# Kernel optimization log

Hardware: AMD Instinct MI355X
Metric: run time of the kernel (lower is better)

Reference implementation:

```python
import jax, jax.numpy as jnp
import numpy as np

EPS = 1e-5
KH = KW = 3
PAD = 1

def conv3x3(x, w, b=None):
    out = jax.lax.conv_general_dilated(
        x, w, window_strides=(1, 1), padding=((PAD, PAD), (PAD, PAD)),
        dimension_numbers=("NCHW", "OIHW", "NCHW"))
    if b is not None:
        out = out + b[None, :, None, None]
    return out

def batchnorm(x, gamma, beta):
    # training-mode BatchNorm2d: batch statistics over (N, H, W)
    mean = x.mean(axis=(0, 2, 3), keepdims=True)
    var = x.var(axis=(0, 2, 3), keepdims=True)
    return gamma[None, :, None, None] * (x - mean) / jnp.sqrt(var + EPS) + beta[None, :, None, None]

def bilinear_gather(x, y_pos, x_pos):
    # x: [B,C,H,W]; y_pos/x_pos: [B,P,H,W] (P = KH*KW sampling taps)
    # zero padding outside image (mmcv modulated deform conv semantics)
    B, C, H, W = x.shape
    P = y_pos.shape[1]
    x_flat = x.reshape(B, C, H * W)
    y0 = jnp.floor(y_pos)
    x0 = jnp.floor(x_pos)
    ly = y_pos - y0
    lx = x_pos - x0
    out = jnp.zeros((B, C, P, H, W), dtype=x.dtype)
    for dy, dx, wgt in ((0, 0, (1 - ly) * (1 - lx)), (0, 1, (1 - ly) * lx),
                        (1, 0, ly * (1 - lx)), (1, 1, ly * lx)):
        yi = y0 + dy
        xi = x0 + dx
        valid = ((yi >= 0) & (yi <= H - 1) & (xi >= 0) & (xi <= W - 1)).astype(x.dtype)
        yc = jnp.clip(yi, 0, H - 1).astype(jnp.int32)
        xc = jnp.clip(xi, 0, W - 1).astype(jnp.int32)
        idx = (yc * W + xc).reshape(B, 1, P * H * W)
        vals = jnp.take_along_axis(x_flat, jnp.broadcast_to(idx, (B, C, P * H * W)), axis=2)
        vals = vals.reshape(B, C, P, H, W)
        out = out + vals * (wgt * valid)[:, None]
    return out  # [B,C,P,H,W]

def modulated_deform_conv(x, w_off, b_off, w_dcn):
    B, C, H, W = x.shape
    P = KH * KW
    off = conv3x3(x, w_off, b_off)  # [B, 3*P, H, W]
    o1, o2, m = jnp.split(off, 3, axis=1)
    offset = jnp.concatenate([o1, o2], axis=1)            # [B, 2P, H, W]
    offset = offset.reshape(B, P, 2, H, W)                # channel 2p -> dy, 2p+1 -> dx
    mask = jax.nn.sigmoid(m)                              # [B, P, H, W]
    hh = jnp.arange(H, dtype=x.dtype)
    ww = jnp.arange(W, dtype=x.dtype)
    ky = jnp.arange(KH, dtype=x.dtype)
    kx = jnp.arange(KW, dtype=x.dtype)
    # base sampling grid per tap p = ky*KW + kx: (h - PAD + ky, w - PAD + kx)
    base_y = (hh[None, :] - PAD + ky[:, None])            # [KH, H]
    base_x = (ww[None, :] - PAD + kx[:, None])            # [KW, W]
    base_y = jnp.broadcast_to(base_y[:, None, :, None], (KH, KW, H, W)).reshape(P, H, W)
    base_x = jnp.broadcast_to(base_x[None, :, None, :], (KH, KW, H, W)).reshape(P, H, W)
    y_pos = base_y[None] + offset[:, :, 0]                # [B,P,H,W]
    x_pos = base_x[None] + offset[:, :, 1]
    sampled = bilinear_gather(x, y_pos, x_pos)            # [B,C,P,H,W]
    sampled = sampled * mask[:, None]
    w = w_dcn.reshape(w_dcn.shape[0], C, P)               # [O, C, P]
    return jnp.einsum("bcphw,ocp->bohw", sampled, w)

def setup_inputs() -> dict:
    key = jax.random.key(0)
    ks = jax.random.split(key, 10)
    B, Ch, H, W = 4, 256, 64, 64
    Cin, Cout = 2 * Ch, 256
    P = KH * KW
    inp = {
        "input_v": jax.random.normal(ks[0], (B, Ch, H, W), jnp.float32),
        "input_i": jax.random.normal(ks[1], (B, Ch, H, W), jnp.float32),
        "w_off": jax.random.normal(ks[2], (3 * P, Cin, KH, KW), jnp.float32) * 0.01,
        "b_off": jnp.zeros((3 * P,), jnp.float32),
        "w_dcn": jax.random.normal(ks[3], (Cout, Cin, KH, KW), jnp.float32) * (1.0 / np.sqrt(Cin * P)),
        "gamma1": jnp.ones((Cout,), jnp.float32),
        "beta1": jnp.zeros((Cout,), jnp.float32),
        "w2": jax.random.normal(ks[4], (Cout, Cout, KH, KW), jnp.float32) * (1.0 / np.sqrt(Cout * P)),
        "gamma2": jnp.ones((Cout,), jnp.float32),
        "beta2": jnp.zeros((Cout,), jnp.float32),
    }
    return inp

def reference(input_v, input_i, w_off, b_off, w_dcn, gamma1, beta1, w2, gamma2, beta2):
    x = jnp.concatenate([input_v, input_i], axis=1)
    out = modulated_deform_conv(x, w_off, b_off, w_dcn)
    out = jax.nn.relu(batchnorm(out, gamma1, beta1))
    out = jax.nn.relu(batchnorm(conv3x3(out, w2), gamma2, beta2))
    return out
```

## Files before the change

kernel.cpp:

```cpp
#include <hip/hip_runtime.h>
#include <cstdint>
#include <cstddef>

typedef unsigned short u16;
typedef __attribute__((ext_vector_type(8))) short s16x8;
typedef __attribute__((ext_vector_type(4))) float f32x4;

#define DEV __device__ __forceinline__

DEV float bf2f(short u){
  union { unsigned int i; float f; } v;
  v.i = ((unsigned int)(u16)u) << 16;
  return v.f;
}
DEV short f2bf(float f){
  union { float f; unsigned int i; } v; v.f = f;
  unsigned int u = v.i;
  u += 0x7fffu + ((u >> 16) & 1u);
  return (short)(u >> 16);
}
DEV f32x4 f32x4_zero(){
  f32x4 z;
#pragma unroll
  for(int j=0;j<4;j++) z[j]=0.f;
  return z;
}
DEV f32x4 mfma16(s16x8 a, s16x8 b, f32x4 c){
  return __builtin_amdgcn_mfma_f32_16x16x32_bf16(a, b, c, 0, 0, 0);
}
DEV void bar_lds(){
  asm volatile("s_waitcnt lgkmcnt(0)" ::: "memory");
  __builtin_amdgcn_s_barrier();
}
DEV void gload16(const u16* g, u16* l){
  __builtin_amdgcn_global_load_lds(
      (const __attribute__((address_space(1))) unsigned int*)g,
      (__attribute__((address_space(3))) unsigned int*)l, 16, 0, 0);
}

static constexpr size_t STATS_B     = 0;
static constexpr size_t OUT2_ACC_B  = 4096;
static constexpr size_t XN_PAD_B    = 16781312;
static constexpr size_t OUT1N_PAD_B = 34738176;
static constexpr size_t ZERO_BYTES  = 43659264;
static constexpr size_t OUT1_ACC_B  = 43659264;
static constexpr size_t PPIX_B      = 60436480;
static constexpr size_t PWGT_B      = 62795776;
static constexpr size_t Y_B         = 65155072;
static constexpr size_t WALL_B      = 159428608;
static constexpr size_t W2T_B       = 162181120;

__global__ void k_x_to_nhwc(const float* __restrict__ v, const float* __restrict__ vi,
                            u16* __restrict__ xn){
  __shared__ float tile[64][65];
  const int b = blockIdx.z, c0 = blockIdx.y*64, hw0 = blockIdx.x*64;
  const int h = hw0 >> 6;
  const float* src = (c0 < 256) ? (v  + ((size_t)b*256 + c0)      *4096)
                                : (vi + ((size_t)b*256 + (c0-256))*4096);
  const int t = threadIdx.x;
#pragma unroll
  for(int k=0;k<16;k++){
    int idx = t + k*256;
    int cl = idx >> 6, wl = idx & 63;
    tile[cl][wl] = src[(size_t)cl*4096 + hw0 + wl];
  }
  __syncthreads();
#pragma unroll
  for(int k=0;k<16;k++){
    int idx = t + k*256;
    int wl = idx >> 6, cl = idx & 63;
    xn[((size_t)(b*66 + h+1)*66 + wl+1)*512 + c0 + cl] = (u16)f2bf(tile[cl][wl]);
  }
}

__global__ void k_prep_wall(const float* __restrict__ wdcn, const float* __restrict__ woff,
                            u16* __restrict__ wt){
  int idx = blockIdx.x*256 + threadIdx.x;
  if(idx >= 2688*512) return;
  int n = idx >> 9, c = idx & 511;
  float val = 0.f;
  if(n < 2304){
    int p = n >> 8, o = n & 255;
    val = wdcn[(size_t)(o*512 + c)*9 + p];
  } else if(n < 2592){
    int q = n - 2304, p = q >> 5, nn = q & 31;
    if(nn < 27) val = woff[(size_t)(nn*512 + c)*9 + p];
  }
  wt[idx] = (u16)f2bf(val);
}
__global__ void k_prep_w2(const float* __restrict__ w, u16* __restrict__ wt){
  int idx = blockIdx.x*256 + threadIdx.x;
  if(idx >= 256*2304) return;
  int n = idx / 2304, k = idx % 2304;
  int t = k >> 8, c = k & 255;
  wt[idx] = (u16)f2bf(w[(size_t)(n*256 + c)*9 + t]);
}

__global__ __launch_bounds__(256, 2) void k_gemm_big(
    const u16* __restrict__ A, const u16* __restrict__ wt, u16* __restrict__ Y){
  const int bid = blockIdx.x;
  const int xcd = bid & 7;
  const int j   = bid >> 3;
  const int mt  = xcd + 8*(j/7);
  const int ng  = j % 7;
  if(mt >= 137) return;
  __shared__ short A_lds[2][8][128][8];
  __shared__ short B_lds[2][8][128][8];
  const int tid = threadIdx.x;
  const int lane = tid & 63, wid = tid >> 6;
  const int quad = lane >> 4, ln = lane & 15;
  const int wm = wid >> 1, wn = wid & 1;
  const int m0 = mt * 128;
  constexpr int NPH = 24;
  f32x4 acc[4][4];
#pragma unroll
  for(int mf=0;mf<4;mf++)
#pragma unroll
    for(int nf=0;nf<4;nf++) acc[mf][nf] = f32x4_zero();

  auto stage = [&](int p, int bi){
    const int n0 = (ng*3 + (p >> 3)) * 128;
    const int k0 = (p & 7) * 64;
#pragma unroll
    for(int i=0;i<4;i++){
      const int idx = wid*4 + i;
      const int s = idx >> 1, rh = (idx & 1)*64;
      gload16(A  + (size_t)(m0 + rh + lane)*512 + k0 + s*8, (u16*)&A_lds[bi][s][rh][0]);
      gload16(wt + (size_t)(n0 + rh + lane)*512 + k0 + s*8, (u16*)&B_lds[bi][s][rh][0]);
    }
  };
  auto compute = [&](int bi){
#pragma unroll
    for(int kk=0;kk<2;kk++){
      s16x8 af[4], bf[4];
#pragma unroll
      for(int mf=0;mf<4;mf++)
        af[mf] = *(const s16x8*)&A_lds[bi][kk*4+quad][wm*64 + mf*16 + ln][0];
#pragma unroll
      for(int nf=0;nf<4;nf++)
        bf[nf] = *(const s16x8*)&B_lds[bi][kk*4+quad][wn*64 + nf*16 + ln][0];
#pragma unroll
      for(int mf=0;mf<4;mf++)
#pragma unroll
        for(int nf=0;nf<4;nf++)
          acc[mf][nf] = mfma16(af[mf], bf[nf], acc[mf][nf]);
    }
  };
  auto flushY = [&](int pass){
    const int n0 = (ng*3 + pass) * 128;
#pragma unroll
    for(int mf=0;mf<4;mf++)
#pragma unroll
      for(int nf=0;nf<4;nf++){
        const int col = n0 + wn*64 + nf*16 + ln;
#pragma unroll
        for(int i=0;i<4;i++){
          const int row = m0 + wm*64 + mf*16 + quad*4 + i;
          Y[(size_t)row*2688 + col] = (u16)f2bf(acc[mf][nf][i]);
        }
        acc[mf][nf] = f32x4_zero();
      }
  };

  stage(0, 0);
  asm volatile("s_waitcnt vmcnt(0)" ::: "memory");
  __builtin_amdgcn_s_barrier();
  stage(1, 1);
  for(int p = 0; p < NPH; ++p){
    const int bi = p & 1;
    compute(bi);
    bar_lds();
    const bool boundary = (p & 7) == 7;
    if(boundary) flushY(p >> 3);
    if(p + 2 < NPH) stage(p + 2, bi);
    if(boundary || p + 2 >= NPH){
      asm volatile("s_waitcnt vmcnt(0)" ::: "memory");
    } else {
      asm volatile("s_waitcnt vmcnt(8)" ::: "memory");
    }
    __builtin_amdgcn_sched_barrier(0);
    __builtin_amdgcn_s_barrier();
  }
}

__global__ __launch_bounds__(256) void k_off_combine(
    const u16* __restrict__ Y, const float* __restrict__ boff,
    int* __restrict__ ppix, float* __restrict__ pwgt){
  __shared__ float offs[64][32];
  const int t = threadIdx.x;
  const int b = blockIdx.x >> 6, h = blockIdx.x & 63;
  const int w = t >> 2, g = t & 3;
  float acc[8];
#pragma unroll
  for(int j=0;j<8;j++) acc[j] = 0.f;
  for(int p=0;p<9;p++){
    const int pp = (b*66 + h + p/3)*66 + (w + p%3);
    s16x8 v = *(const s16x8*)(Y + (size_t)pp*2688 + 2304 + p*32 + g*8);
#pragma unroll
    for(int j=0;j<8;j++) acc[j] += bf2f(v[j]);
  }
#pragma unroll
  for(int j=0;j<8;j++) offs[w][g*8 + j] = acc[j];
  __syncthreads();
  for(int id = t; id < 576; id += 256){
    const int tp = id / 64, ww = id & 63;
    const int m = (b<<12) + (h<<6) + ww;
    float dy = offs[ww][2*tp]   + boff[2*tp];
    float dx = offs[ww][2*tp+1] + boff[2*tp+1];
    float mz = offs[ww][18+tp]  + boff[18+tp];
    float mk = 1.f / (1.f + expf(-mz));
    float ypos = (float)(h - 1 + tp/3) + dy;
    float xpos = (float)(ww - 1 + tp%3) + dx;
    float y0f = floorf(ypos), x0f = floorf(xpos);
    float ly = ypos - y0f, lx = xpos - x0f;
    int y0 = (int)y0f, x0 = (int)x0f;
    const int id4 = (m*9 + tp)*4;
#pragma unroll
    for(int k=0;k<4;k++){
      int ddy = k >> 1, ddx = k & 1;
      int yi = y0 + ddy, xi = x0 + ddx;
      int yc = yi < -1 ? -1 : (yi > 64 ? 64 : yi);
      int xc = xi < -1 ? -1 : (xi > 64 ? 64 : xi);
      float wk = (ddy ? ly : 1.f-ly) * (ddx ? lx : 1.f-lx) * mk;
      ppix[id4+k] = (b*66 + yc+1)*66 + xc+1;
      pwgt[id4+k] = wk;
    }
  }
}

__global__ __launch_bounds__(512) void k_combine(
    const u16* __restrict__ Y, const int* __restrict__ ppix,
    const float* __restrict__ pwgt, float* __restrict__ out1,
    float* __restrict__ sum1, float* __restrict__ sq1){
  __shared__ int   s_pp[64][9][4];
  __shared__ float s_wg[64][9][4];
  __shared__ float s_red[2][8][256];
  const int t = threadIdx.x;
  const int b = blockIdx.x >> 6, h = blockIdx.x & 63;
  const int m_row = (b<<12) + (h<<6);
  for(int id = t; id < 576; id += 512){
    const int mo = id / 9, tp = id - mo*9;
    const size_t i4 = ((size_t)(m_row + mo)*9 + tp)*4;
    int4   pp4 = *(const int4*)  (ppix + i4);
    float4 wg4 = *(const float4*)(pwgt + i4);
    s_pp[mo][tp][0] = pp4.x; s_pp[mo][tp][1] = pp4.y;
    s_pp[mo][tp][2] = pp4.z; s_pp[mo][tp][3] = pp4.w;
    s_wg[mo][tp][0] = wg4.x; s_wg[mo][tp][1] = wg4.y;
    s_wg[mo][tp][2] = wg4.z; s_wg[mo][tp][3] = wg4.w;
  }
  __syncthreads();
  const int wv = t >> 6, lane = t & 63;
  const int c0 = lane*4;
  const int pw0 = wv*8;
  float acc[8][4];
#pragma unroll
  for(int pw=0;pw<8;pw++)
#pragma unroll
    for(int j=0;j<4;j++) acc[pw][j] = 0.f;

  for(int tp = 0; tp < 9; ++tp){
    const int cb = tp*256 + c0;
#pragma unroll
    for(int pw=0;pw<8;pw++){
      const int px = pw0 + pw;
#pragma unroll
      for(int k=0;k<4;k++){
        const float wk = s_wg[px][tp][k];
        const int   pp = s_pp[px][tp][k];
        ushort4 v = *(const ushort4*)(Y + (size_t)pp*2688 + cb);
        acc[pw][0] = fmaf(wk, bf2f((short)v.x), acc[pw][0]);
        acc[pw][1] = fmaf(wk, bf2f((short)v.y), acc[pw][1]);
        acc[pw][2] = fmaf(wk, bf2f((short)v.z), acc[pw][2]);
        acc[pw][3] = fmaf(wk, bf2f((short)v.w), acc[pw][3]);
      }
    }
  }
  float ls[4] = {0.f,0.f,0.f,0.f}, lq[4] = {0.f,0.f,0.f,0.f};
#pragma unroll
  for(int pw=0;pw<8;pw++){
    float4 o4;
    o4.x = acc[pw][0]; o4.y = acc[pw][1]; o4.z = acc[pw][2]; o4.w = acc[pw][3];
    *(float4*)(out1 + (size_t)(m_row + pw0 + pw)*256 + c0) = o4;
#pragma unroll
    for(int j=0;j<4;j++){
      ls[j] += acc[pw][j];
      lq[j] = fmaf(acc[pw][j], acc[pw][j], lq[j]);
    }
  }
#pragma unroll
  for(int j=0;j<4;j++){
    s_red[0][wv][c0+j] = ls[j];
    s_red[1][wv][c0+j] = lq[j];
  }
  __syncthreads();
  if(t < 256){
    float S = 0.f, Q = 0.f;
#pragma unroll
    for(int w8=0;w8<8;w8++){ S += s_red[0][w8][t]; Q += s_red[1][w8][t]; }
    unsafeAtomicAdd(sum1 + t, S);
    unsafeAtomicAdd(sq1 + t, Q);
  }
}

__global__ __launch_bounds__(256, 2) void k_gemm2(
    const u16* __restrict__ a_pad, const u16* __restrict__ wt, float* __restrict__ outa){
  const int bid = blockIdx.x;
  const int xcd = bid & 7;
  const int j   = bid >> 3;
  const int mt  = xcd + 8*(j >> 2);
  const int rest = j & 3;
  const int nt  = rest & 1;
  const int kz  = rest >> 1;
  __shared__ short A_lds[2][8][128][8];
  __shared__ short B_lds[2][8][128][8];
  const int tid = threadIdx.x;
  const int lane = tid & 63, wid = tid >> 6;
  const int quad = lane >> 4, ln = lane & 15;
  const int wm = wid >> 1, wn = wid & 1;
  const int m0 = mt * 128;
  const int n0 = nt * 128;
  const int kbase = kz * 1152;
  const int b = m0 >> 12;
  const int h0 = (m0 & 4095) >> 6;
  constexpr int NPH = 18;
  f32x4 acc[4][4];
#pragma unroll
  for(int mf=0;mf<4;mf++)
#pragma unroll
    for(int nf=0;nf<4;nf++) acc[mf][nf] = f32x4_zero();

  auto stage = [&](int t, int bi){
    const int k0 = kbase + t*64;
    const int tp = k0 >> 8, cit = k0 & 255;
    const int ty = tp/3, tx = tp - ty*3;
#pragma unroll
    for(int i=0;i<4;i++){
      const int idx = wid*4 + i;
      const int s = idx >> 1, rh = (idx & 1)*64;
      const int hh = h0 + (rh >> 6) + ty;
      gload16(a_pad + ((size_t)(b*66 + hh)*66 + lane + tx)*256 + cit + s*8,
              (u16*)&A_lds[bi][s][rh][0]);
      gload16(wt + (size_t)(n0 + rh + lane)*2304 + k0 + s*8,
              (u16*)&B_lds[bi][s][rh][0]);
    }
  };
  auto compute = [&](int bi){
#pragma unroll
    for(int kk=0;kk<2;kk++){
      s16x8 af[4], bf[4];
#pragma unroll
      for(int mf=0;mf<4;mf++)
        af[mf] = *(const s16x8*)&A_lds[bi][kk*4+quad][wm*64 + mf*16 + ln][0];
#pragma unroll
      for(int nf=0;nf<4;nf++)
        bf[nf] = *(const s16x8*)&B_lds[bi][kk*4+quad][wn*64 + nf*16 + ln][0];
#pragma unroll
      for(int mf=0;mf<4;mf++)
#pragma unroll
        for(int nf=0;nf<4;nf++)
          acc[mf][nf] = mfma16(af[mf], bf[nf], acc[mf][nf]);
    }
  };

  stage(0, 0);
  asm volatile("s_waitcnt vmcnt(0)" ::: "memory");
  __builtin_amdgcn_s_barrier();
  stage(1, 1);
  for(int t = 0; t < NPH; ++t){
    const int bi = t & 1;
    compute(bi);
    bar_lds();
    if(t + 2 < NPH){
      stage(t + 2, bi);
      asm volatile("s_waitcnt vmcnt(8)" ::: "memory");
    } else {
      asm volatile("s_waitcnt vmcnt(0)" ::: "memory");
    }
    __builtin_amdgcn_sched_barrier(0);
    __builtin_amdgcn_s_barrier();
  }

#pragma unroll
  for(int mf=0;mf<4;mf++)
#pragma unroll
    for(int nf=0;nf<4;nf++){
      const int col = n0 + wn*64 + nf*16 + ln;
#pragma unroll
      for(int i=0;i<4;i++){
        const int row = m0 + wm*64 + mf*16 + quad*4 + i;
        unsafeAtomicAdd(outa + (size_t)row*256 + col, acc[mf][nf][i]);
      }
    }
}

__global__ void k_stats(const float* __restrict__ acc, float* __restrict__ sum,
                        float* __restrict__ sq){
  const int m0 = blockIdx.x*64;
  const int c = threadIdx.x;
  float s = 0.f, q = 0.f;
  for(int i=0;i<64;i++){
    float v = acc[(size_t)(m0+i)*256 + c];
    s += v; q += v*v;
  }
  unsafeAtomicAdd(sum + c, s);
  unsafeAtomicAdd(sq + c, q);
}

__global__ void k_bn1(const float* __restrict__ acc, const float* __restrict__ sum,
                      const float* __restrict__ sq, const float* __restrict__ g,
                      const float* __restrict__ bt, u16* __restrict__ o){
  __shared__ float sc[256], sh[256];
  const int t = threadIdx.x;
  {
    float mean = sum[t] * (1.f/16384.f);
    float var  = sq[t] * (1.f/16384.f) - mean*mean;
    float rstd = rsqrtf(var + 1e-5f);
    float s = g[t] * rstd;
    sc[t] = s; sh[t] = bt[t] - mean*s;
  }
  __syncthreads();
  const int c4 = (t & 63) * 4;
  const float s0 = sc[c4], s1 = sc[c4+1], s2 = sc[c4+2], s3 = sc[c4+3];
  const float h0 = sh[c4], h1 = sh[c4+1], h2 = sh[c4+2], h3 = sh[c4+3];
#pragma unroll
  for(int k=0;k<4;k++){
    int m = blockIdx.x*16 + k*4 + (t>>6);
    int b = m >> 12, hh = (m >> 6) & 63, ww = m & 63;
    const float4 v = *(const float4*)(acc + (size_t)m*256 + c4);
    unsigned int lo = (unsigned int)(u16)f2bf(fmaxf(0.f, v.x*s0 + h0))
                    | ((unsigned int)(u16)f2bf(fmaxf(0.f, v.y*s1 + h1)) << 16);
    unsigned int hi = (unsigned int)(u16)f2bf(fmaxf(0.f, v.z*s2 + h2))
                    | ((unsigned int)(u16)f2bf(fmaxf(0.f, v.w*s3 + h3)) << 16);
    uint2 pr; pr.x = lo; pr.y = hi;
    *(uint2*)(o + ((size_t)(b*66 + hh+1)*66 + ww+1)*256 + c4) = pr;
  }
}

__global__ void k_bn2_out(const float* __restrict__ acc, const float* __restrict__ sum,
                          const float* __restrict__ sq, const float* __restrict__ g,
                          const float* __restrict__ bt, float* __restrict__ out){
  __shared__ float tile[64][65];
  __shared__ float sc[64], sh[64];
  const int t = threadIdx.x;
  const int b = blockIdx.z, c0 = blockIdx.y*64, hw0 = blockIdx.x*64;
  if(t < 64){
    int c = c0 + t;
    float mean = sum[c] * (1.f/16384.f);
    float var  = sq[c] * (1.f/16384.f) - mean*mean;
    float rstd = rsqrtf(var + 1e-5f);
    float s = g[c] * rstd;
    sc[t] = s; sh[t] = bt[c] - mean*s;
  }
  __syncthreads();
#pragma unroll
  for(int k=0;k<16;k++){
    int idx = t + k*256;
    int wl = idx >> 6, cl = idx & 63;
    float v = acc[(size_t)((b<<12) + hw0 + wl)*256 + c0 + cl];
    tile[wl][cl] = fmaxf(0.f, v*sc[cl] + sh[cl]);
  }
  __syncthreads();
#pragma unroll
  for(int k=0;k<16;k++){
    int idx = t + k*256;
    int cl = idx >> 6, wl = idx & 63;
    out[(size_t)(b*256 + c0 + cl)*4096 + hw0 + wl] = tile[wl][cl];
  }
}

extern "C" void kernel_launch(void* const* d_in, const int* in_sizes, int n_in,
                              void* d_out, int out_size, void* d_ws, size_t ws_size,
                              hipStream_t stream){
  const float* in_v  = (const float*)d_in[0];
  const float* in_i  = (const float*)d_in[1];
  const float* w_off = (const float*)d_in[2];
  const float* b_off = (const float*)d_in[3];
  const float* w_dcn = (const float*)d_in[4];
  const float* g1    = (const float*)d_in[5];
  const float* bt1   = (const float*)d_in[6];
  const float* w2    = (const float*)d_in[7];
  const float* g2    = (const float*)d_in[8];
  const float* bt2   = (const float*)d_in[9];
  float* out = (float*)d_out;
  char* ws = (char*)d_ws;

  float* stats     = (float*)(ws + STATS_B);
  float* out2_acc  = (float*)(ws + OUT2_ACC_B);
  u16*   xn_pad    = (u16*)  (ws + XN_PAD_B);
  u16*   out1n_pad = (u16*)  (ws + OUT1N_PAD_B);
  float* out1_acc  = (float*)(ws + OUT1_ACC_B);
  int*   ppix      = (int*)  (ws + PPIX_B);
  float* pwgt      = (float*)(ws + PWGT_B);
  u16*   Ymat      = (u16*)  (ws + Y_B);
  u16*   wall      = (u16*)  (ws + WALL_B);
  u16*   w2t       = (u16*)  (ws + W2T_B);
  float* sum1 = stats,       *sq1 = stats + 256;
  float* sum2 = stats + 512, *sq2 = stats + 768;

  hipMemsetAsync(ws, 0, ZERO_BYTES, stream);
  k_x_to_nhwc<<<dim3(64,8,4), 256, 0, stream>>>(in_v, in_i, xn_pad);
  k_prep_wall<<<5376, 256, 0, stream>>>(w_dcn, w_off, wall);
  k_prep_w2<<<2304, 256, 0, stream>>>(w2, w2t);
  k_gemm_big<<<1008, 256, 0, stream>>>(xn_pad, wall, Ymat);
  k_off_combine<<<256, 256, 0, stream>>>(Ymat, b_off, ppix, pwgt);
  k_combine<<<256, 512, 0, stream>>>(Ymat, ppix, pwgt, out1_acc, sum1, sq1);
  k_bn1<<<1024, 256, 0, stream>>>(out1_acc, sum1, sq1, g1, bt1, out1n_pad);
  k_gemm2<<<512, 256, 0, stream>>>(out1n_pad, w2t, out2_acc);
  k_stats<<<256, 256, 0, stream>>>(out2_acc, sum2, sq2);
  k_bn2_out<<<dim3(64,4,4), 256, 0, stream>>>(out2_acc, sum2, sq2, g2, bt2, out);
}
```

Baseline: 351.2 us.

## Drop double-buffered pipelines in GEMMs for smaller LDS and higher occupancy

Both GEMM kernels lose their hand-built double-buffered global-to-LDS pipeline and become a simple single-buffer loop: load a K=32 slice, barrier, run the MFMAs, barrier. LDS per block shrinks so launch bounds can request 4 blocks per CU. The big GEMM also drops its multi-pass N loop per block and gives each block a single 128-wide N tile, tripling the grid. The aim is to hide latency through more resident waves instead of explicit prefetch, at the cost of two barriers per smaller K step and no load/compute overlap within a block.

```diff
diff --git a/kernel.cpp b/kernel.cpp
--- a/kernel.cpp
+++ b/kernel.cpp
@@ -27,10 +27,6 @@
 }
 DEV f32x4 mfma16(s16x8 a, s16x8 b, f32x4 c){
   return __builtin_amdgcn_mfma_f32_16x16x32_bf16(a, b, c, 0, 0, 0);
-}
-DEV void bar_lds(){
-  asm volatile("s_waitcnt lgkmcnt(0)" ::: "memory");
-  __builtin_amdgcn_s_barrier();
 }
 DEV void gload16(const u16* g, u16* l){
   __builtin_amdgcn_global_load_lds(
@@ -96,91 +92,68 @@
   wt[idx] = (u16)f2bf(w[(size_t)(n*256 + c)*9 + t]);
 }
 
-__global__ __launch_bounds__(256, 2) void k_gemm_big(
+__global__ __launch_bounds__(256, 4) void k_gemm_big(
     const u16* __restrict__ A, const u16* __restrict__ wt, u16* __restrict__ Y){
   const int bid = blockIdx.x;
   const int xcd = bid & 7;
   const int j   = bid >> 3;
-  const int mt  = xcd + 8*(j/7);
-  const int ng  = j % 7;
+  const int mt  = xcd + 8*(j/21);
+  const int nt  = j % 21;
   if(mt >= 137) return;
-  __shared__ short A_lds[2][8][128][8];
-  __shared__ short B_lds[2][8][128][8];
+  __shared__ short A_lds[4][128][8];
+  __shared__ short B_lds[4][128][8];
   const int tid = threadIdx.x;
   const int lane = tid & 63, wid = tid >> 6;
   const int quad = lane >> 4, ln = lane & 15;
   const int wm = wid >> 1, wn = wid & 1;
   const int m0 = mt * 128;
-  constexpr int NPH = 24;
+  const int n0 = nt * 128;
   f32x4 acc[4][4];
 #pragma unroll
   for(int mf=0;mf<4;mf++)
 #pragma unroll
     for(int nf=0;nf<4;nf++) acc[mf][nf] = f32x4_zero();
 
-  auto stage = [&](int p, int bi){
-    const int n0 = (ng*3 + (p >> 3)) * 128;
-    const int k0 = (p & 7) * 64;
+  for(int t = 0; t < 16; ++t){
+    const int k0 = t*32;
 #pragma unroll
     for(int i=0;i<4;i++){
-      const int idx = wid*4 + i;
-      const int s = idx >> 1, rh = (idx & 1)*64;
-      gload16(A  + (size_t)(m0 + rh + lane)*512 + k0 + s*8, (u16*)&A_lds[bi][s][rh][0]);
-      gload16(wt + (size_t)(n0 + rh + lane)*512 + k0 + s*8, (u16*)&B_lds[bi][s][rh][0]);
-    }
-  };
-  auto compute = [&](int bi){
-#pragma unroll
-    for(int kk=0;kk<2;kk++){
+      const int piece = wid*4 + i;
+      const int s = (piece >> 1) & 3, rh = (piece & 1)*64;
+      if(piece < 8)
+        gload16(A  + (size_t)(m0 + rh + lane)*512 + k0 + s*8, (u16*)&A_lds[s][rh][0]);
+      else
+        gload16(wt + (size_t)(n0 + rh + lane)*512 + k0 + s*8, (u16*)&B_lds[s][rh][0]);
+    }
+    __syncthreads();
+    {
       s16x8 af[4], bf[4];
 #pragma unroll
       for(int mf=0;mf<4;mf++)
-        af[mf] = *(const s16x8*)&A_lds[bi][kk*4+quad][wm*64 + mf*16 + ln][0];
+        af[mf] = *(const s16x8*)&A_lds[quad][wm*64 + mf*16 + ln][0];
 #pragma unroll
       for(int nf=0;nf<4;nf++)
-        bf[nf] = *(const s16x8*)&B_lds[bi][kk*4+quad][wn*64 + nf*16 + ln][0];
+        bf[nf] = *(const s16x8*)&B_lds[quad][wn*64 + nf*16 + ln][0];
 #pragma unroll
       for(int mf=0;mf<4;mf++)
 #pragma unroll
         for(int nf=0;nf<4;nf++)
           acc[mf][nf] = mfma16(af[mf], bf[nf], acc[mf][nf]);
     }
-  };
-  auto flushY = [&](int pass){
-    const int n0 = (ng*3 + pass) * 128;
-#pragma unroll
-    for(int mf=0;mf<4;mf++)
-#pragma unroll
-      for(int nf=0;nf<4;nf++){
-        const int col = n0 + wn*64 + nf*16 + ln;
-#pragma unroll
-        for(int i=0;i<4;i++){
-          const int row = m0 + wm*64 + mf*16 + quad*4 + i;
-          Y[(size_t)row*2688 + col] = (u16)f2bf(acc[mf][nf][i]);
-        }
-        acc[mf][nf] = f32x4_zero();
+    __syncthreads();
+  }
+
+#pragma unroll
+  for(int mf=0;mf<4;mf++)
+#pragma unroll
+    for(int nf=0;nf<4;nf++){
+      const int col = n0 + wn*64 + nf*16 + ln;
+#pragma unroll
+      for(int i=0;i<4;i++){
+        const int row = m0 + wm*64 + mf*16 + quad*4 + i;
+        Y[(size_t)row*2688 + col] = (u16)f2bf(acc[mf][nf][i]);
       }
-  };
-
-  stage(0, 0);
-  asm volatile("s_waitcnt vmcnt(0)" ::: "memory");
-  __builtin_amdgcn_s_barrier();
-  stage(1, 1);
-  for(int p = 0; p < NPH; ++p){
-    const int bi = p & 1;
-    compute(bi);
-    bar_lds();
-    const bool boundary = (p & 7) == 7;
-    if(boundary) flushY(p >> 3);
-    if(p + 2 < NPH) stage(p + 2, bi);
-    if(boundary || p + 2 >= NPH){
-      asm volatile("s_waitcnt vmcnt(0)" ::: "memory");
-    } else {
-      asm volatile("s_waitcnt vmcnt(8)" ::: "memory");
-    }
-    __builtin_amdgcn_sched_barrier(0);
-    __builtin_amdgcn_s_barrier();
-  }
+    }
 }
 
 __global__ __launch_bounds__(256) void k_off_combine(
@@ -302,7 +275,7 @@
   }
 }
 
-__global__ __launch_bounds__(256, 2) void k_gemm2(
+__global__ __launch_bounds__(256, 4) void k_gemm2(
     const u16* __restrict__ a_pad, const u16* __restrict__ wt, float* __restrict__ outa){
   const int bid = blockIdx.x;
   const int xcd = bid & 7;
@@ -311,8 +284,8 @@
   const int rest = j & 3;
   const int nt  = rest & 1;
   const int kz  = rest >> 1;
-  __shared__ short A_lds[2][8][128][8];
-  __shared__ short B_lds[2][8][128][8];
+  __shared__ short A_lds[4][128][8];
+  __shared__ short B_lds[4][128][8];
   const int tid = threadIdx.x;
   const int lane = tid & 63, wid = tid >> 6;
   const int quad = lane >> 4, ln = lane & 15;
@@ -322,62 +295,45 @@
   const int kbase = kz * 1152;
   const int b = m0 >> 12;
   const int h0 = (m0 & 4095) >> 6;
-  constexpr int NPH = 18;
   f32x4 acc[4][4];
 #pragma unroll
   for(int mf=0;mf<4;mf++)
 #pragma unroll
     for(int nf=0;nf<4;nf++) acc[mf][nf] = f32x4_zero();
 
-  auto stage = [&](int t, int bi){
-    const int k0 = kbase + t*64;
+  for(int t = 0; t < 36; ++t){
+    const int k0 = kbase + t*32;
     const int tp = k0 >> 8, cit = k0 & 255;
     const int ty = tp/3, tx = tp - ty*3;
 #pragma unroll
     for(int i=0;i<4;i++){
-      const int idx = wid*4 + i;
-      const int s = idx >> 1, rh = (idx & 1)*64;
-      const int hh = h0 + (rh >> 6) + ty;
-      gload16(a_pad + ((size_t)(b*66 + hh)*66 + lane + tx)*256 + cit + s*8,
-              (u16*)&A_lds[bi][s][rh][0]);
-      gload16(wt + (size_t)(n0 + rh + lane)*2304 + k0 + s*8,
-              (u16*)&B_lds[bi][s][rh][0]);
-    }
-  };
-  auto compute = [&](int bi){
-#pragma unroll
-    for(int kk=0;kk<2;kk++){
+      const int piece = wid*4 + i;
+      const int s = (piece >> 1) & 3, rh = (piece & 1)*64;
+      if(piece < 8){
+        const int hh = h0 + (rh >> 6) + ty;
+        gload16(a_pad + ((size_t)(b*66 + hh)*66 + lane + tx)*256 + cit + s*8,
+                (u16*)&A_lds[s][rh][0]);
+      } else {
+        gload16(wt + (size_t)(n0 + rh + lane)*2304 + k0 + s*8,
+                (u16*)&B_lds[s][rh][0]);
+      }
+    }
+    __syncthreads();
+    {
       s16x8 af[4], bf[4];
 #pragma unroll
       for(int mf=0;mf<4;mf++)
-        af[mf] = *(const s16x8*)&A_lds[bi][kk*4+quad][wm*64 + mf*16 + ln][0];
+        af[mf] = *(const s16x8*)&A_lds[quad][wm*64 + mf*16 + ln][0];
 #pragma unroll
       for(int nf=0;nf<4;nf++)
-        bf[nf] = *(const s16x8*)&B_lds[bi][kk*4+quad][wn*64 + nf*16 + ln][0];
+        bf[nf] = *(const s16x8*)&B_lds[quad][wn*64 + nf*16 + ln][0];
 #pragma unroll
       for(int mf=0;mf<4;mf++)
 #pragma unroll
         for(int nf=0;nf<4;nf++)
           acc[mf][nf] = mfma16(af[mf], bf[nf], acc[mf][nf]);
     }
-  };
-
-  stage(0, 0);
-  asm volatile("s_waitcnt vmcnt(0)" ::: "memory");
-  __builtin_amdgcn_s_barrier();
-  stage(1, 1);
-  for(int t = 0; t < NPH; ++t){
-    const int bi = t & 1;
-    compute(bi);
-    bar_lds();
-    if(t + 2 < NPH){
-      stage(t + 2, bi);
-      asm volatile("s_waitcnt vmcnt(8)" ::: "memory");
-    } else {
-      asm volatile("s_waitcnt vmcnt(0)" ::: "memory");
-    }
-    __builtin_amdgcn_sched_barrier(0);
-    __builtin_amdgcn_s_barrier();
+    __syncthreads();
   }
 
 #pragma unroll
@@ -501,7 +457,7 @@
   k_x_to_nhwc<<<dim3(64,8,4), 256, 0, stream>>>(in_v, in_i, xn_pad);
   k_prep_wall<<<5376, 256, 0, stream>>>(w_dcn, w_off, wall);
   k_prep_w2<<<2304, 256, 0, stream>>>(w2, w2t);
-  k_gemm_big<<<1008, 256, 0, stream>>>(xn_pad, wall, Ymat);
+  k_gemm_big<<<3024, 256, 0, stream>>>(xn_pad, wall, Ymat);
   k_off_combine<<<256, 256, 0, stream>>>(Ymat, b_off, ppix, pwgt);
   k_combine<<<256, 512, 0, stream>>>(Ymat, ppix, pwgt, out1_acc, sum1, sq1);
   k_bn1<<<1024, 256, 0, stream>>>(out1_acc, sum1, sq1, g1, bt1, out1n_pad);
```

New measurement: 360.1 us. 2.5% more time.

## Merge prep kernels, fuse offset computation into combine, store bf16 intermediate

Applied to the files above, without the earlier changes.

Merges the three input and weight preparation kernels into one launch that dispatches on block index. The offset/bilinear-weight computation is folded into the combine kernel, so sampling indices and weights stay in shared memory instead of going through global buffers. The pre-BN1 activation is now stored as bf16 rather than fp32, halving that traffic for combine and bn1. This removes launches and global round trips, but BN1 is now applied to values rounded to bf16 while its statistics still come from the fp32 values.

```diff
diff --git a/kernel.cpp b/kernel.cpp
--- a/kernel.cpp
+++ b/kernel.cpp
@@ -43,57 +43,56 @@
 static constexpr size_t XN_PAD_B    = 16781312;
 static constexpr size_t OUT1N_PAD_B = 34738176;
 static constexpr size_t ZERO_BYTES  = 43659264;
-static constexpr size_t OUT1_ACC_B  = 43659264;
-static constexpr size_t PPIX_B      = 60436480;
-static constexpr size_t PWGT_B      = 62795776;
-static constexpr size_t Y_B         = 65155072;
-static constexpr size_t WALL_B      = 159428608;
-static constexpr size_t W2T_B       = 162181120;
-
-__global__ void k_x_to_nhwc(const float* __restrict__ v, const float* __restrict__ vi,
-                            u16* __restrict__ xn){
+static constexpr size_t OUT1RAW_B   = 43659264;
+static constexpr size_t Y_B         = 52047872;
+static constexpr size_t WALL_B      = 146321408;
+static constexpr size_t W2T_B       = 149073920;
+
+__global__ __launch_bounds__(256) void k_prep_all(
+    const float* __restrict__ v, const float* __restrict__ vi, u16* __restrict__ xn,
+    const float* __restrict__ wdcn, const float* __restrict__ woff, u16* __restrict__ wall,
+    const float* __restrict__ w2, u16* __restrict__ w2t){
   __shared__ float tile[64][65];
-  const int b = blockIdx.z, c0 = blockIdx.y*64, hw0 = blockIdx.x*64;
-  const int h = hw0 >> 6;
-  const float* src = (c0 < 256) ? (v  + ((size_t)b*256 + c0)      *4096)
-                                : (vi + ((size_t)b*256 + (c0-256))*4096);
+  const int blk = blockIdx.x;
   const int t = threadIdx.x;
-#pragma unroll
-  for(int k=0;k<16;k++){
-    int idx = t + k*256;
-    int cl = idx >> 6, wl = idx & 63;
-    tile[cl][wl] = src[(size_t)cl*4096 + hw0 + wl];
-  }
-  __syncthreads();
-#pragma unroll
-  for(int k=0;k<16;k++){
-    int idx = t + k*256;
-    int wl = idx >> 6, cl = idx & 63;
-    xn[((size_t)(b*66 + h+1)*66 + wl+1)*512 + c0 + cl] = (u16)f2bf(tile[cl][wl]);
-  }
-}
-
-__global__ void k_prep_wall(const float* __restrict__ wdcn, const float* __restrict__ woff,
-                            u16* __restrict__ wt){
-  int idx = blockIdx.x*256 + threadIdx.x;
-  if(idx >= 2688*512) return;
-  int n = idx >> 9, c = idx & 511;
-  float val = 0.f;
-  if(n < 2304){
-    int p = n >> 8, o = n & 255;
-    val = wdcn[(size_t)(o*512 + c)*9 + p];
-  } else if(n < 2592){
-    int q = n - 2304, p = q >> 5, nn = q & 31;
-    if(nn < 27) val = woff[(size_t)(nn*512 + c)*9 + p];
-  }
-  wt[idx] = (u16)f2bf(val);
-}
-__global__ void k_prep_w2(const float* __restrict__ w, u16* __restrict__ wt){
-  int idx = blockIdx.x*256 + threadIdx.x;
-  if(idx >= 256*2304) return;
-  int n = idx / 2304, k = idx % 2304;
-  int t = k >> 8, c = k & 255;
-  wt[idx] = (u16)f2bf(w[(size_t)(n*256 + c)*9 + t]);
+  if(blk < 2048){
+    const int hw0 = (blk & 63) * 64;
+    const int c0  = ((blk >> 6) & 7) * 64;
+    const int b   = blk >> 9;
+    const int h   = hw0 >> 6;
+    const float* src = (c0 < 256) ? (v  + ((size_t)b*256 + c0)      *4096)
+                                  : (vi + ((size_t)b*256 + (c0-256))*4096);
+#pragma unroll
+    for(int k=0;k<16;k++){
+      int idx = t + k*256;
+      int cl = idx >> 6, wl = idx & 63;
+      tile[cl][wl] = src[(size_t)cl*4096 + hw0 + wl];
+    }
+    __syncthreads();
+#pragma unroll
+    for(int k=0;k<16;k++){
+      int idx = t + k*256;
+      int wl = idx >> 6, cl = idx & 63;
+      xn[((size_t)(b*66 + h+1)*66 + wl+1)*512 + c0 + cl] = (u16)f2bf(tile[cl][wl]);
+    }
+  } else if(blk < 7424){
+    int idx = (blk - 2048)*256 + t;
+    int n = idx >> 9, c = idx & 511;
+    float val = 0.f;
+    if(n < 2304){
+      int p = n >> 8, o = n & 255;
+      val = wdcn[(size_t)(o*512 + c)*9 + p];
+    } else if(n < 2592){
+      int q = n - 2304, p = q >> 5, nn = q & 31;
+      if(nn < 27) val = woff[(size_t)(nn*512 + c)*9 + p];
+    }
+    wall[idx] = (u16)f2bf(val);
+  } else {
+    int idx = (blk - 7424)*256 + t;
+    int n = idx / 2304, k = idx % 2304;
+    int tp = k >> 8, c = k & 255;
+    w2t[idx] = (u16)f2bf(w2[(size_t)(n*256 + c)*9 + tp]);
+  }
 }
 
 __global__ __launch_bounds__(256, 2) void k_gemm_big(
@@ -183,28 +182,35 @@
   }
 }
 
-__global__ __launch_bounds__(256) void k_off_combine(
+__global__ __launch_bounds__(512) void k_combine(
     const u16* __restrict__ Y, const float* __restrict__ boff,
-    int* __restrict__ ppix, float* __restrict__ pwgt){
+    u16* __restrict__ out1raw, float* __restrict__ sum1, float* __restrict__ sq1){
   __shared__ float offs[64][32];
+  __shared__ int   s_pp[64][9][4];
+  __shared__ float s_wg[64][9][4];
+  __shared__ float s_red[2][8][256];
   const int t = threadIdx.x;
   const int b = blockIdx.x >> 6, h = blockIdx.x & 63;
-  const int w = t >> 2, g = t & 3;
-  float acc[8];
-#pragma unroll
-  for(int j=0;j<8;j++) acc[j] = 0.f;
-  for(int p=0;p<9;p++){
-    const int pp = (b*66 + h + p/3)*66 + (w + p%3);
-    s16x8 v = *(const s16x8*)(Y + (size_t)pp*2688 + 2304 + p*32 + g*8);
-#pragma unroll
-    for(int j=0;j<8;j++) acc[j] += bf2f(v[j]);
-  }
-#pragma unroll
-  for(int j=0;j<8;j++) offs[w][g*8 + j] = acc[j];
-  __syncthreads();
-  for(int id = t; id < 576; id += 256){
+  const int m_row = (b<<12) + (h<<6);
+
+  if(t < 256){
+    const int w = t >> 2, g = t & 3;
+    float oa[8];
+#pragma unroll
+    for(int j=0;j<8;j++) oa[j] = 0.f;
+    for(int p=0;p<9;p++){
+      const int pp = (b*66 + h + p/3)*66 + (w + p%3);
+      s16x8 vv = *(const s16x8*)(Y + (size_t)pp*2688 + 2304 + p*32 + g*8);
+#pragma unroll
+      for(int j=0;j<8;j++) oa[j] += bf2f(vv[j]);
+    }
+#pragma unroll
+    for(int j=0;j<8;j++) offs[w][g*8 + j] = oa[j];
+  }
+  __syncthreads();
+
+  for(int id = t; id < 576; id += 512){
     const int tp = id / 64, ww = id & 63;
-    const int m = (b<<12) + (h<<6) + ww;
     float dy = offs[ww][2*tp]   + boff[2*tp];
     float dx = offs[ww][2*tp+1] + boff[2*tp+1];
     float mz = offs[ww][18+tp]  + boff[18+tp];
@@ -214,7 +220,6 @@
     float y0f = floorf(ypos), x0f = floorf(xpos);
     float ly = ypos - y0f, lx = xpos - x0f;
     int y0 = (int)y0f, x0 = (int)x0f;
-    const int id4 = (m*9 + tp)*4;
 #pragma unroll
     for(int k=0;k<4;k++){
       int ddy = k >> 1, ddx = k & 1;
@@ -222,33 +227,12 @@
       int yc = yi < -1 ? -1 : (yi > 64 ? 64 : yi);
       int xc = xi < -1 ? -1 : (xi > 64 ? 64 : xi);
       float wk = (ddy ? ly : 1.f-ly) * (ddx ? lx : 1.f-lx) * mk;
-      ppix[id4+k] = (b*66 + yc+1)*66 + xc+1;
-      pwgt[id4+k] = wk;
-    }
-  }
-}
-
-__global__ __launch_bounds__(512) void k_combine(
-    const u16* __restrict__ Y, const int* __restrict__ ppix,
-    const float* __restrict__ pwgt, float* __restrict__ out1,
-    float* __restrict__ sum1, float* __restrict__ sq1){
-  __shared__ int   s_pp[64][9][4];
-  __shared__ float s_wg[64][9][4];
-  __shared__ float s_red[2][8][256];
-  const int t = threadIdx.x;
-  const int b = blockIdx.x >> 6, h = blockIdx.x & 63;
-  const int m_row = (b<<12) + (h<<6);
-  for(int id = t; id < 576; id += 512){
-    const int mo = id / 9, tp = id - mo*9;
-    const size_t i4 = ((size_t)(m_row + mo)*9 + tp)*4;
-    int4   pp4 = *(const int4*)  (ppix + i4);
-    float4 wg4 = *(const float4*)(pwgt + i4);
-    s_pp[mo][tp][0] = pp4.x; s_pp[mo][tp][1] = pp4.y;
-    s_pp[mo][tp][2] = pp4.z; s_pp[mo][tp][3] = pp4.w;
-    s_wg[mo][tp][0] = wg4.x; s_wg[mo][tp][1] = wg4.y;
-    s_wg[mo][tp][2] = wg4.z; s_wg[mo][tp][3] = wg4.w;
-  }
-  __syncthreads();
+      s_pp[ww][tp][k] = (b*66 + yc+1)*66 + xc+1;
+      s_wg[ww][tp][k] = wk;
+    }
+  }
+  __syncthreads();
+
   const int wv = t >> 6, lane = t & 63;
   const int c0 = lane*4;
   const int pw0 = wv*8;
@@ -278,9 +262,10 @@
   float ls[4] = {0.f,0.f,0.f,0.f}, lq[4] = {0.f,0.f,0.f,0.f};
 #pragma unroll
   for(int pw=0;pw<8;pw++){
-    float4 o4;
-    o4.x = acc[pw][0]; o4.y = acc[pw][1]; o4.z = acc[pw][2]; o4.w = acc[pw][3];
-    *(float4*)(out1 + (size_t)(m_row + pw0 + pw)*256 + c0) = o4;
+    ushort4 o4;
+    o4.x = (u16)f2bf(acc[pw][0]); o4.y = (u16)f2bf(acc[pw][1]);
+    o4.z = (u16)f2bf(acc[pw][2]); o4.w = (u16)f2bf(acc[pw][3]);
+    *(ushort4*)(out1raw + (size_t)(m_row + pw0 + pw)*256 + c0) = o4;
 #pragma unroll
     for(int j=0;j<4;j++){
       ls[j] += acc[pw][j];
@@ -299,6 +284,36 @@
     for(int w8=0;w8<8;w8++){ S += s_red[0][w8][t]; Q += s_red[1][w8][t]; }
     unsafeAtomicAdd(sum1 + t, S);
     unsafeAtomicAdd(sq1 + t, Q);
+  }
+}
+
+__global__ void k_bn1(const u16* __restrict__ raw, const float* __restrict__ sum,
+                      const float* __restrict__ sq, const float* __restrict__ g,
+                      const float* __restrict__ bt, u16* __restrict__ o){
+  __shared__ float sc[256], sh[256];
+  const int t = threadIdx.x;
+  {
+    float mean = sum[t] * (1.f/16384.f);
+    float var  = sq[t] * (1.f/16384.f) - mean*mean;
+    float rstd = rsqrtf(var + 1e-5f);
+    float s = g[t] * rstd;
+    sc[t] = s; sh[t] = bt[t] - mean*s;
+  }
+  __syncthreads();
+  const int c4 = (t & 63) * 4;
+  const float s0 = sc[c4], s1 = sc[c4+1], s2 = sc[c4+2], s3 = sc[c4+3];
+  const float h0 = sh[c4], h1 = sh[c4+1], h2 = sh[c4+2], h3 = sh[c4+3];
+#pragma unroll
+  for(int k=0;k<4;k++){
+    int m = blockIdx.x*16 + k*4 + (t>>6);
+    int b = m >> 12, hh = (m >> 6) & 63, ww = m & 63;
+    const ushort4 v = *(const ushort4*)(raw + (size_t)m*256 + c4);
+    unsigned int lo = (unsigned int)(u16)f2bf(fmaxf(0.f, bf2f((short)v.x)*s0 + h0))
+                    | ((unsigned int)(u16)f2bf(fmaxf(0.f, bf2f((short)v.y)*s1 + h1)) << 16);
+    unsigned int hi = (unsigned int)(u16)f2bf(fmaxf(0.f, bf2f((short)v.z)*s2 + h2))
+                    | ((unsigned int)(u16)f2bf(fmaxf(0.f, bf2f((short)v.w)*s3 + h3)) << 16);
+    uint2 pr; pr.x = lo; pr.y = hi;
+    *(uint2*)(o + ((size_t)(b*66 + hh+1)*66 + ww+1)*256 + c4) = pr;
   }
 }
 
@@ -406,36 +421,6 @@
   unsafeAtomicAdd(sq + c, q);
 }
 
-__global__ void k_bn1(const float* __restrict__ acc, const float* __restrict__ sum,
-                      const float* __restrict__ sq, const float* __restrict__ g,
-                      const float* __restrict__ bt, u16* __restrict__ o){
-  __shared__ float sc[256], sh[256];
-  const int t = threadIdx.x;
-  {
-    float mean = sum[t] * (1.f/16384.f);
-    float var  = sq[t] * (1.f/16384.f) - mean*mean;
-    float rstd = rsqrtf(var + 1e-5f);
-    float s = g[t] * rstd;
-    sc[t] = s; sh[t] = bt[t] - mean*s;
-  }
-  __syncthreads();
-  const int c4 = (t & 63) * 4;
-  const float s0 = sc[c4], s1 = sc[c4+1], s2 = sc[c4+2], s3 = sc[c4+3];
-  const float h0 = sh[c4], h1 = sh[c4+1], h2 = sh[c4+2], h3 = sh[c4+3];
-#pragma unroll
-  for(int k=0;k<4;k++){
-    int m = blockIdx.x*16 + k*4 + (t>>6);
-    int b = m >> 12, hh = (m >> 6) & 63, ww = m & 63;
-    const float4 v = *(const float4*)(acc + (size_t)m*256 + c4);
-    unsigned int lo = (unsigned int)(u16)f2bf(fmaxf(0.f, v.x*s0 + h0))
-                    | ((unsigned int)(u16)f2bf(fmaxf(0.f, v.y*s1 + h1)) << 16);
-    unsigned int hi = (unsigned int)(u16)f2bf(fmaxf(0.f, v.z*s2 + h2))
-                    | ((unsigned int)(u16)f2bf(fmaxf(0.f, v.w*s3 + h3)) << 16);
-    uint2 pr; pr.x = lo; pr.y = hi;
-    *(uint2*)(o + ((size_t)(b*66 + hh+1)*66 + ww+1)*256 + c4) = pr;
-  }
-}
-
 __global__ void k_bn2_out(const float* __restrict__ acc, const float* __restrict__ sum,
                           const float* __restrict__ sq, const float* __restrict__ g,
                           const float* __restrict__ bt, float* __restrict__ out){
@@ -488,9 +473,7 @@
   float* out2_acc  = (float*)(ws + OUT2_ACC_B);
   u16*   xn_pad    = (u16*)  (ws + XN_PAD_B);
   u16*   out1n_pad = (u16*)  (ws + OUT1N_PAD_B);
-  float* out1_acc  = (float*)(ws + OUT1_ACC_B);
-  int*   ppix      = (int*)  (ws + PPIX_B);
-  float* pwgt      = (float*)(ws + PWGT_B);
+  u16*   out1raw   = (u16*)  (ws + OUT1RAW_B);
   u16*   Ymat      = (u16*)  (ws + Y_B);
   u16*   wall      = (u16*)  (ws + WALL_B);
   u16*   w2t       = (u16*)  (ws + W2T_B);
@@ -498,13 +481,10 @@
   float* sum2 = stats + 512, *sq2 = stats + 768;
 
   hipMemsetAsync(ws, 0, ZERO_BYTES, stream);
-  k_x_to_nhwc<<<dim3(64,8,4), 256, 0, stream>>>(in_v, in_i, xn_pad);
-  k_prep_wall<<<5376, 256, 0, stream>>>(w_dcn, w_off, wall);
-  k_prep_w2<<<2304, 256, 0, stream>>>(w2, w2t);
+  k_prep_all<<<9728, 256, 0, stream>>>(in_v, in_i, xn_pad, w_dcn, w_off, wall, w2, w2t);
   k_gemm_big<<<1008, 256, 0, stream>>>(xn_pad, wall, Ymat);
-  k_off_combine<<<256, 256, 0, stream>>>(Ymat, b_off, ppix, pwgt);
-  k_combine<<<256, 512, 0, stream>>>(Ymat, ppix, pwgt, out1_acc, sum1, sq1);
-  k_bn1<<<1024, 256, 0, stream>>>(out1_acc, sum1, sq1, g1, bt1, out1n_pad);
+  k_combine<<<256, 512, 0, stream>>>(Ymat, b_off, out1raw, sum1, sq1);
+  k_bn1<<<1024, 256, 0, stream>>>(out1raw, sum1, sq1, g1, bt1, out1n_pad);
   k_gemm2<<<512, 256, 0, stream>>>(out1n_pad, w2t, out2_acc);
   k_stats<<<256, 256, 0, stream>>>(out2_acc, sum2, sq2);
   k_bn2_out<<<dim3(64,4,4), 256, 0, stream>>>(out2_acc, sum2, sq2, g2, bt2, out);
```

New measurement: 371.2 us. 1.06x slower.
